# Performance work log

Hardware: AMD Instinct MI355X
Metric: run time of the kernel (lower is better)

Reference implementation:

```python
import jax, jax.numpy as jnp
import numpy as np

N, IN_DIM, HEADS, OUT_DIM, EDGE_DIM = 3072, 128, 4, 64, 8
EPS = 1e-5


def setup_inputs() -> dict:
    key = jax.random.key(0)
    ks = jax.random.split(key, 8)
    x = jax.random.normal(ks[0], (N, IN_DIM), dtype=jnp.float32)
    adj = jax.random.randint(ks[1], (N, N), 0, 2, dtype=jnp.int32)
    edge_feats = jax.random.normal(ks[2], (N, N, EDGE_DIM), dtype=jnp.float32)
    W = jax.random.normal(ks[3], (IN_DIM, HEADS * OUT_DIM), dtype=jnp.float32) * (IN_DIM ** -0.5)
    a_src = jax.random.normal(ks[4], (HEADS, OUT_DIM), dtype=jnp.float32) * 0.01
    a_dst = jax.random.normal(ks[5], (HEADS, OUT_DIM), dtype=jnp.float32) * 0.01
    ep_w = jax.random.normal(ks[6], (EDGE_DIM, HEADS), dtype=jnp.float32) * (EDGE_DIM ** -0.5)
    ep_b = jax.random.normal(ks[7], (HEADS,), dtype=jnp.float32) * 0.01
    gamma = jnp.ones((HEADS * OUT_DIM,), dtype=jnp.float32)
    beta = jnp.zeros((HEADS * OUT_DIM,), dtype=jnp.float32)
    return {"x": x, "adj": adj, "edge_feats": edge_feats, "W": W, "a_src": a_src,
            "a_dst": a_dst, "ep_w": ep_w, "ep_b": ep_b, "gamma": gamma, "beta": beta}


def reference(x, adj, edge_feats, W, a_src, a_dst, ep_w, ep_b, gamma, beta):
    n = x.shape[0]
    h = (x @ W).reshape(n, HEADS, OUT_DIM)                      # (N,H,D)
    s_src = jnp.einsum('nhd,hd->nh', h, a_src)                  # (N,H)
    s_dst = jnp.einsum('nhd,hd->nh', h, a_dst)                  # (N,H)
    edge_attn = jnp.einsum('ije,eh->ijh', edge_feats, ep_w) + ep_b  # (N,N,H)
    attn = s_src[:, None, :] + s_dst[None, :, :] + edge_attn    # (N,N,H)
    attn = jax.nn.leaky_relu(attn, 0.2)
    neg = jnp.finfo(attn.dtype).min
    attn = jnp.where((adj == 0)[:, :, None], neg, attn)
    attn = jax.nn.softmax(attn, axis=1)                         # softmax over neighbors j
    # dropout is identity in eval mode
    out = jnp.einsum('ijh,jhd->ihd', attn, h).reshape(n, HEADS * OUT_DIM)
    mean = out.mean(-1, keepdims=True)
    var = out.var(-1, keepdims=True)
    out = (out - mean) * jax.lax.rsqrt(var + EPS) * gamma + beta
    return out
```

## Files before the change

### kernel.cpp

```cpp
#include <hip/hip_runtime.h>

#define NN     3072
#define INDIM  128
#define NH     4
#define DD     64
#define CC     256
#define EE     8
#define NODE_T 8
#define TI16   16
#define BJ     64
#define JSPLIT 4
#define JRANGE (NN / JSPLIT)
#define NTS    (JRANGE / BJ)
#define PTJ    72
#define NCH    (NN / 32)

typedef short short8v __attribute__((ext_vector_type(8)));
typedef unsigned short ushort8v __attribute__((ext_vector_type(8)));
typedef float float4v __attribute__((ext_vector_type(4)));

__device__ __forceinline__ float bf2f(unsigned short u) {
    return __uint_as_float(((unsigned int)u) << 16);
}
__device__ __forceinline__ unsigned short f2bf(float f) {
    unsigned int u = __float_as_uint(f);
    u += 0x7fffu + ((u >> 16) & 1u);
    return (unsigned short)(u >> 16);
}
__device__ __forceinline__ float rfl(float f) {
    return __int_as_float(__builtin_amdgcn_readfirstlane(__float_as_int(f)));
}

__global__ __launch_bounds__(256) void hproj(
    const float* __restrict__ x,
    const float* __restrict__ W,
    const float* __restrict__ a_src,
    const float* __restrict__ a_dst,
    unsigned short* __restrict__ htf,
    float* __restrict__ s_src,
    float* __restrict__ s_dst)
{
    const int tid = threadIdx.x;
    const int n0  = blockIdx.x * NODE_T;
    const int h   = tid >> 6, lane = tid & 63;

    float acc[NODE_T] = {};
#pragma unroll 4
    for (int k = 0; k < INDIM; ++k) {
        const float wv = W[(size_t)k * CC + tid];
#pragma unroll
        for (int n = 0; n < NODE_T; ++n)
            acc[n] = fmaf(x[(size_t)(n0 + n) * INDIM + k], wv, acc[n]);
    }

    ushort8v hv;
#pragma unroll
    for (int n = 0; n < NODE_T; ++n) hv[n] = f2bf(acc[n]);
    unsigned short* dst = htf
        + (size_t)((h * 4 + (lane >> 4)) * NCH + (n0 >> 5)) * 512
        + (size_t)((((n0 >> 3) & 3) * 16 + (lane & 15)) * 8);
    *reinterpret_cast<ushort8v*>(dst) = hv;

    const float asv = a_src[h * DD + lane];
    const float adv = a_dst[h * DD + lane];
#pragma unroll
    for (int n = 0; n < NODE_T; ++n) {
        float s1 = acc[n] * asv, s2 = acc[n] * adv;
#pragma unroll
        for (int off = 32; off > 0; off >>= 1) {
            s1 += __shfl_xor(s1, off, 64);
            s2 += __shfl_xor(s2, off, 64);
        }
        if (lane == 0) {
            s_src[(size_t)(n0 + n) * NH + h] = s1;
            s_dst[(size_t)(n0 + n) * NH + h] = s2;
        }
    }
}

__global__ __launch_bounds__(256, 3) void gat_fused(
    const int* __restrict__ adj,
    const float* __restrict__ ef,
    const unsigned short* __restrict__ htf,
    const float* __restrict__ s_src,
    const float* __restrict__ s_dst,
    const float* __restrict__ ep_w,
    const float* __restrict__ ep_b,
    float* __restrict__ out_part,
    float* __restrict__ l_part)
{
    __shared__ unsigned short pt[2][NH][16][PTJ];

    const int tid  = threadIdx.x;
    const int rw   = tid >> 6;
    const int lane = tid & 63;
    const int l15  = lane & 15;
    const int q    = lane >> 4;
    const int bid  = blockIdx.x;
    const int s    = bid & (JSPLIT - 1);
    const int i0   = (bid >> 2) * TI16;
    const int jb0  = s * JRANGE;

    float epw[EE][NH], epb4[NH];
#pragma unroll
    for (int e = 0; e < EE; ++e)
#pragma unroll
        for (int h = 0; h < NH; ++h) epw[e][h] = ep_w[e * NH + h];
#pragma unroll
    for (int h = 0; h < NH; ++h) epb4[h] = ep_b[h];
    float ssrc[4][4];
#pragma unroll
    for (int r = 0; r < 4; ++r)
#pragma unroll
        for (int h = 0; h < NH; ++h)
            ssrc[r][h] = rfl(s_src[(size_t)(i0 + rw * 4 + r) * NH + h]);

    float4v acc[4];
#pragma unroll
    for (int f = 0; f < 4; ++f) acc[f] = (float4v){0.f, 0.f, 0.f, 0.f};
    float l_loc[4][4] = {};

    float4 efA[4], efB[4], sd4;
    int    ajr[4];

#define LOADP(JN) {                                                          \
        const int jj = (JN) + lane;                                          \
        sd4 = *reinterpret_cast<const float4*>(s_dst + (size_t)jj * NH);     \
        _Pragma("unroll")                                                    \
        for (int r = 0; r < 4; ++r) {                                        \
            const size_t ro = (size_t)(i0 + rw * 4 + r) * NN;                \
            ajr[r] = adj[ro + jj];                                           \
            const float* ep = ef + (ro + jj) * EE;                           \
            efA[r] = *reinterpret_cast<const float4*>(ep);                   \
            efB[r] = *reinterpret_cast<const float4*>(ep + 4);               \
        } }

#define SCOREP(NB) {                                                         \
        const float sdh[4] = {sd4.x, sd4.y, sd4.z, sd4.w};                   \
        _Pragma("unroll")                                                    \
        for (int r = 0; r < 4; ++r) {                                        \
            const float ev[EE] = {efA[r].x, efA[r].y, efA[r].z, efA[r].w,    \
                                  efB[r].x, efB[r].y, efB[r].z, efB[r].w};   \
            _Pragma("unroll")                                                \
            for (int h = 0; h < NH; ++h) {                                   \
                float sc = ssrc[r][h] + sdh[h] + epb4[h];                    \
                _Pragma("unroll")                                            \
                for (int e = 0; e < EE; ++e)                                 \
                    sc = fmaf(ev[e], epw[e][h], sc);                         \
                sc = (sc > 0.f) ? sc : 0.2f * sc;                            \
                const float p = (ajr[r] == 0) ? 0.f : __expf(sc);            \
                const unsigned short bb = f2bf(p);                           \
                l_loc[r][h] += bf2f(bb);                                     \
                pt[NB][h][rw * 4 + r][lane] = bb;                            \
            } } }

    LOADP(jb0);
    SCOREP(0);
    __syncthreads();

    int buf = 0;
    for (int t = 0; t < NTS; ++t) {
        const int jb   = jb0 + t * BJ;
        const int cid0 = jb >> 5;
        const bool pf  = (t + 1 < NTS);

        short8v bfrag[2][4];
#pragma unroll
        for (int ks = 0; ks < 2; ++ks)
#pragma unroll
            for (int f = 0; f < 4; ++f)
                bfrag[ks][f] = *reinterpret_cast<const short8v*>(
                    htf + (size_t)((rw * 4 + f) * NCH + cid0 + ks) * 512 + lane * 8);
        __builtin_amdgcn_sched_barrier(0);

        if (pf) LOADP(jb + BJ);
        __builtin_amdgcn_sched_barrier(0);

#pragma unroll
        for (int ks = 0; ks < 2; ++ks) {
            const short8v a = *reinterpret_cast<const short8v*>(
                &pt[buf][rw][l15][ks * 32 + q * 8]);
#pragma unroll
            for (int f = 0; f < 4; ++f)
                acc[f] = __builtin_amdgcn_mfma_f32_16x16x32_bf16(a, bfrag[ks][f], acc[f], 0, 0, 0);
        }

        if (pf) SCOREP(buf ^ 1);
        __syncthreads();
        buf ^= 1;
    }

#pragma unroll
    for (int r = 0; r < 4; ++r)
#pragma unroll
        for (int h = 0; h < NH; ++h) {
            float v = l_loc[r][h];
#pragma unroll
            for (int off = 32; off > 0; off >>= 1) v += __shfl_xor(v, off, 64);
            if (lane == 0)
                l_part[((size_t)s * NN + i0 + rw * 4 + r) * NH + h] = v;
        }

#pragma unroll
    for (int f = 0; f < 4; ++f)
#pragma unroll
        for (int rg = 0; rg < 4; ++rg)
            out_part[((size_t)s * NN + i0 + q * 4 + rg) * CC + rw * DD + f * 16 + l15] = acc[f][rg];
#undef LOADP
#undef SCOREP
}

__global__ __launch_bounds__(256) void gat_ln(
    const float* __restrict__ out_part,
    const float* __restrict__ l_part,
    const float* __restrict__ gamma,
    const float* __restrict__ beta,
    float* __restrict__ out)
{
    const int tid = threadIdx.x, w = tid >> 6, lane = tid & 63;
    const int i = blockIdx.x * 4 + w;

    float v[4];
#pragma unroll
    for (int k = 0; k < 4; ++k) {
        float a = 0.f;
#pragma unroll
        for (int sp = 0; sp < JSPLIT; ++sp)
            a += out_part[((size_t)sp * NN + i) * CC + k * 64 + lane];
        float lb = 0.f;
#pragma unroll
        for (int sp = 0; sp < JSPLIT; ++sp)
            lb += l_part[((size_t)sp * NN + i) * NH + k];
        v[k] = a / lb;
    }

    float s1 = v[0] + v[1] + v[2] + v[3];
    float s2 = v[0] * v[0] + v[1] * v[1] + v[2] * v[2] + v[3] * v[3];
#pragma unroll
    for (int off = 32; off > 0; off >>= 1) {
        s1 += __shfl_xor(s1, off, 64);
        s2 += __shfl_xor(s2, off, 64);
    }
    const float mean = s1 * (1.f / CC);
    const float var  = s2 * (1.f / CC) - mean * mean;
    const float rstd = rsqrtf(var + 1e-5f);
    float* op = out + (size_t)i * CC;
#pragma unroll
    for (int k = 0; k < 4; ++k) {
        const int c = k * 64 + lane;
        op[c] = (v[k] - mean) * rstd * gamma[c] + beta[c];
    }
}

extern "C" void kernel_launch(void* const* d_in, const int* in_sizes, int n_in,
                              void* d_out, int out_size, void* d_ws, size_t ws_size,
                              hipStream_t stream) {
    const float* x     = (const float*)d_in[0];
    const int*   adj   = (const int*)d_in[1];
    const float* ef    = (const float*)d_in[2];
    const float* W     = (const float*)d_in[3];
    const float* a_src = (const float*)d_in[4];
    const float* a_dst = (const float*)d_in[5];
    const float* ep_w  = (const float*)d_in[6];
    const float* ep_b  = (const float*)d_in[7];
    const float* gamma = (const float*)d_in[8];
    const float* beta  = (const float*)d_in[9];

    float* s_src = (float*)d_ws;
    float* s_dst = s_src + (size_t)NN * NH;
    unsigned short* htf = (unsigned short*)(s_dst + (size_t)NN * NH);
    float* out_part = (float*)(htf + (size_t)NN * CC);
    float* l_part   = out_part + (size_t)JSPLIT * NN * CC;
    (void)ws_size; (void)in_sizes; (void)n_in; (void)out_size;

    hipLaunchKernelGGL(hproj, dim3(NN / NODE_T), dim3(256), 0, stream,
                       x, W, a_src, a_dst, htf, s_src, s_dst);
    hipLaunchKernelGGL(gat_fused, dim3((NN / TI16) * JSPLIT), dim3(256), 0, stream,
                       adj, ef, htf, s_src, s_dst, ep_w, ep_b, out_part, l_part);
    hipLaunchKernelGGL(gat_ln, dim3(NN / 4), dim3(256), 0, stream,
                       out_part, l_part, gamma, beta, (float*)d_out);
}
```

Baseline: 472.1 us.

## Deepen edge-feature prefetch to two tiles ahead with dual register sets

The attention kernel now keeps two register sets of edge features, adjacency and s_dst, and loads the tile two steps ahead instead of one, so global loads have a full extra iteration to arrive before they are scored. The tile loop is fully unrolled so the register-set choice is resolved at compile time, and ep_b is folded into the per-row s_src constant. This adds register pressure (twice the prefetch registers) and code size, which could reduce occupancy or cause spills.

```diff
diff --git a/kernel.cpp b/kernel.cpp
--- a/kernel.cpp
+++ b/kernel.cpp
@@ -101,68 +101,66 @@
     const int i0   = (bid >> 2) * TI16;
     const int jb0  = s * JRANGE;
 
-    float epw[EE][NH], epb4[NH];
+    float epw[EE][NH];
 #pragma unroll
     for (int e = 0; e < EE; ++e)
 #pragma unroll
-        for (int h = 0; h < NH; ++h) epw[e][h] = ep_w[e * NH + h];
-#pragma unroll
-    for (int h = 0; h < NH; ++h) epb4[h] = ep_b[h];
-    float ssrc[4][4];
+        for (int h = 0; h < NH; ++h) epw[e][h] = rfl(ep_w[e * NH + h]);
+    float sb[4][NH];
 #pragma unroll
     for (int r = 0; r < 4; ++r)
 #pragma unroll
         for (int h = 0; h < NH; ++h)
-            ssrc[r][h] = rfl(s_src[(size_t)(i0 + rw * 4 + r) * NH + h]);
+            sb[r][h] = rfl(s_src[(size_t)(i0 + rw * 4 + r) * NH + h] + ep_b[h]);
 
     float4v acc[4];
 #pragma unroll
     for (int f = 0; f < 4; ++f) acc[f] = (float4v){0.f, 0.f, 0.f, 0.f};
     float l_loc[4][4] = {};
 
-    float4 efA[4], efB[4], sd4;
-    int    ajr[4];
-
-#define LOADP(JN) {                                                          \
+    float4 efA0[4], efB0[4], sd0; int aj0[4];
+    float4 efA1[4], efB1[4], sd1; int aj1[4];
+
+#define LOADP(S, JN) do {                                                    \
         const int jj = (JN) + lane;                                          \
-        sd4 = *reinterpret_cast<const float4*>(s_dst + (size_t)jj * NH);     \
+        sd##S = *reinterpret_cast<const float4*>(s_dst + (size_t)jj * NH);   \
         _Pragma("unroll")                                                    \
         for (int r = 0; r < 4; ++r) {                                        \
             const size_t ro = (size_t)(i0 + rw * 4 + r) * NN;                \
-            ajr[r] = adj[ro + jj];                                           \
+            aj##S[r] = adj[ro + jj];                                         \
             const float* ep = ef + (ro + jj) * EE;                           \
-            efA[r] = *reinterpret_cast<const float4*>(ep);                   \
-            efB[r] = *reinterpret_cast<const float4*>(ep + 4);               \
-        } }
-
-#define SCOREP(NB) {                                                         \
-        const float sdh[4] = {sd4.x, sd4.y, sd4.z, sd4.w};                   \
+            efA##S[r] = *reinterpret_cast<const float4*>(ep);                \
+            efB##S[r] = *reinterpret_cast<const float4*>(ep + 4);            \
+        } } while (0)
+
+#define SCOREP(S, NB) do {                                                   \
+        const float sdh[4] = {sd##S.x, sd##S.y, sd##S.z, sd##S.w};           \
         _Pragma("unroll")                                                    \
         for (int r = 0; r < 4; ++r) {                                        \
-            const float ev[EE] = {efA[r].x, efA[r].y, efA[r].z, efA[r].w,    \
-                                  efB[r].x, efB[r].y, efB[r].z, efB[r].w};   \
+            const float ev[EE] = {efA##S[r].x, efA##S[r].y, efA##S[r].z,     \
+                                  efA##S[r].w, efB##S[r].x, efB##S[r].y,     \
+                                  efB##S[r].z, efB##S[r].w};                 \
             _Pragma("unroll")                                                \
             for (int h = 0; h < NH; ++h) {                                   \
-                float sc = ssrc[r][h] + sdh[h] + epb4[h];                    \
+                float sc = sb[r][h] + sdh[h];                                \
                 _Pragma("unroll")                                            \
                 for (int e = 0; e < EE; ++e)                                 \
                     sc = fmaf(ev[e], epw[e][h], sc);                         \
                 sc = (sc > 0.f) ? sc : 0.2f * sc;                            \
-                const float p = (ajr[r] == 0) ? 0.f : __expf(sc);            \
+                const float p = (aj##S[r] == 0) ? 0.f : __expf(sc);          \
                 const unsigned short bb = f2bf(p);                           \
                 l_loc[r][h] += bf2f(bb);                                     \
                 pt[NB][h][rw * 4 + r][lane] = bb;                            \
-            } } }
-
-    LOADP(jb0);
-    SCOREP(0);
+            } } } while (0)
+
+    LOADP(0, jb0);
+    LOADP(1, jb0 + BJ);
+    SCOREP(0, 0);
     __syncthreads();
 
-    int buf = 0;
+#pragma unroll
     for (int t = 0; t < NTS; ++t) {
-        const int jb   = jb0 + t * BJ;
-        const int cid0 = jb >> 5;
-        const bool pf  = (t + 1 < NTS);
+        const int cid0 = (jb0 + t * BJ) >> 5;
 
         short8v bfrag[2][4];
 #pragma unroll
@@ -173,22 +171,29 @@
                     htf + (size_t)((rw * 4 + f) * NCH + cid0 + ks) * 512 + lane * 8);
         __builtin_amdgcn_sched_barrier(0);
 
-        if (pf) LOADP(jb + BJ);
+        if (t + 2 < NTS) {
+            if ((t & 1) == 0) LOADP(0, jb0 + (t + 2) * BJ);
+            else              LOADP(1, jb0 + (t + 2) * BJ);
+        }
         __builtin_amdgcn_sched_barrier(0);
 
 #pragma unroll
         for (int ks = 0; ks < 2; ++ks) {
             const short8v a = *reinterpret_cast<const short8v*>(
-                &pt[buf][rw][l15][ks * 32 + q * 8]);
+                &pt[t & 1][rw][l15][ks * 32 + q * 8]);
 #pragma unroll
             for (int f = 0; f < 4; ++f)
                 acc[f] = __builtin_amdgcn_mfma_f32_16x16x32_bf16(a, bfrag[ks][f], acc[f], 0, 0, 0);
         }
 
-        if (pf) SCOREP(buf ^ 1);
+        if (t + 1 < NTS) {
+            if ((t & 1) == 0) SCOREP(1, 1);
+            else              SCOREP(0, 0);
+        }
         __syncthreads();
-        buf ^= 1;
-    }
+    }
+#undef LOADP
+#undef SCOREP
 
 #pragma unroll
     for (int r = 0; r < 4; ++r)
@@ -206,8 +211,6 @@
 #pragma unroll
         for (int rg = 0; rg < 4; ++rg)
             out_part[((size_t)s * NN + i0 + q * 4 + rg) * CC + rw * DD + f * 16 + l15] = acc[f][rg];
-#undef LOADP
-#undef SCOREP
 }
 
 __global__ __launch_bounds__(256) void gat_ln(
```

After: 531.5 us. 1.13x slower.
